# Performance work log

Hardware: AMD Instinct MI355X
Metric: run time of the kernel (lower is better)

The kernel has to match this reference:

```python
import jax, jax.numpy as jnp
import numpy as np

GROUPS = 32
EPS = 1e-5


def group_norm(x, gamma, beta):
    B, C, D, H, W = x.shape
    xr = x.reshape(B, GROUPS, C // GROUPS, D, H, W)
    mean = xr.mean(axis=(2, 3, 4, 5), keepdims=True)
    var = xr.var(axis=(2, 3, 4, 5), keepdims=True)
    xn = (xr - mean) * jax.lax.rsqrt(var + EPS)
    xn = xn.reshape(B, C, D, H, W)
    return xn * gamma[None, :, None, None, None] + beta[None, :, None, None, None]


def conv1x1(h, w, b):
    # 1x1x1 Conv3d == channel matmul. w: [O, C], b: [O]
    return jnp.einsum('oc,bcdhw->bodhw', w, h) + b[None, :, None, None, None]


def setup_inputs() -> dict:
    key = jax.random.key(0)
    ks = jax.random.split(key, 10)
    B, C, D, H, W = 2, 128, 16, 16, 16
    x = jax.random.normal(ks[0], (B, C, D, H, W), dtype=jnp.float32)
    gn_w = jnp.ones((C,), dtype=jnp.float32)
    gn_b = jnp.zeros((C,), dtype=jnp.float32)
    # xavier_uniform for [C, C, 1, 1, 1] conv: fan_in = fan_out = C
    lim = float(np.sqrt(6.0 / (C + C)))
    wq = jax.random.uniform(ks[1], (C, C), jnp.float32, -lim, lim)
    wk = jax.random.uniform(ks[2], (C, C), jnp.float32, -lim, lim)
    wv = jax.random.uniform(ks[3], (C, C), jnp.float32, -lim, lim)
    wp = jax.random.uniform(ks[4], (C, C), jnp.float32, -lim, lim) * 1e-05
    bq = jnp.zeros((C,), jnp.float32)
    bk = jnp.zeros((C,), jnp.float32)
    bv = jnp.zeros((C,), jnp.float32)
    bp = jnp.zeros((C,), jnp.float32)
    return {"x": x, "gn_w": gn_w, "gn_b": gn_b, "wq": wq, "bq": bq,
            "wk": wk, "bk": bk, "wv": wv, "bv": bv, "wp": wp, "bp": bp}


def reference(x, gn_w, gn_b, wq, bq, wk, bk, wv, bv, wp, bp):
    B, C, D, H, W = x.shape
    N = D * H * W
    h = group_norm(x, gn_w, gn_b)
    q = conv1x1(h, wq, bq)
    k = conv1x1(h, wk, bk)
    v = conv1x1(h, wv, bv)
    q = q.transpose(0, 2, 3, 4, 1).reshape(B, N, C)   # [B, N, C]
    k = k.reshape(B, C, N)                            # [B, C, N]
    v = v.transpose(0, 2, 3, 4, 1).reshape(B, N, C)   # [B, N, C]
    w = jnp.einsum('bnc,bcm->bnm', q, k) * (C ** -0.5)  # [B, N, N]
    w = jax.nn.softmax(w, axis=-1)
    h = jnp.einsum('bnm,bmc->bnc', w, v)              # [B, N, C]
    h = h.reshape(B, D, H, W, C).transpose(0, 4, 1, 2, 3)
    h = conv1x1(h, wp, bp)
    return x + h
```

## Files before the change

### kernel.cpp

```cpp
#include <hip/hip_runtime.h>
#include <math.h>

#define CC 128
#define NN 4096
#define BB 2
#define NGROUPS 32
#define CPG 4
#define GSIZE (CPG*NN)
#define KSPLIT 2

typedef __attribute__((ext_vector_type(8))) __bf16 bf16x8;
typedef __attribute__((ext_vector_type(4))) float floatx4;

__device__ __forceinline__ unsigned short f2bf(float f) {
  union { float f; unsigned u; } v; v.f = f;
  unsigned r = v.u + 0x7fff + ((v.u >> 16) & 1);
  return (unsigned short)(r >> 16);
}
__device__ __forceinline__ float bf2f(unsigned short u) {
  return __uint_as_float(((unsigned)u) << 16);
}


__global__ void gn_stats_kernel(const float* __restrict__ x, float2* __restrict__ stats) {
  int bid = blockIdx.x;
  int t = threadIdx.x;
  const float4* base = (const float4*)(x + (size_t)bid * 4096);
  float4 v = base[t];
  float s  = v.x + v.y + v.z + v.w;
  float ss = v.x*v.x + v.y*v.y + v.z*v.z + v.w*v.w;
  #pragma unroll
  for (int off = 1; off < 64; off <<= 1) {
    s  += __shfl_xor(s, off);
    ss += __shfl_xor(ss, off);
  }
  __shared__ float sred[4], ssred[4];
  if ((t & 63) == 0) { sred[t >> 6] = s; ssred[t >> 6] = ss; }
  __syncthreads();
  if (t == 0)
    stats[bid] = make_float2(sred[0]+sred[1]+sred[2]+sred[3],
                             ssred[0]+ssred[1]+ssred[2]+ssred[3]);
}

__global__ void prep_kernel(const float2* __restrict__ stats,
                            const float* __restrict__ gamma, const float* __restrict__ beta,
                            const float* __restrict__ wq, const float* __restrict__ bq,
                            const float* __restrict__ wk, const float* __restrict__ wv,
                            const float* __restrict__ wp,
                            float* __restrict__ ab_a, float* __restrict__ ab_b,
                            float* __restrict__ bqs,
                            unsigned short* __restrict__ wqb, unsigned short* __restrict__ wkb,
                            unsigned short* __restrict__ wvb, unsigned short* __restrict__ wpb) {
  const float sc = 0.08838834764831845f;
  int t = threadIdx.x;
  if (blockIdx.x == 64) {
    if (t < BB*NGROUPS) {
      float su = 0.f, ssq = 0.f;
      #pragma unroll
      for (int j = 0; j < 4; j++) { float2 p = stats[t*4 + j]; su += p.x; ssq += p.y; }
      float mean = su * (1.0f/GSIZE);
      float var  = ssq * (1.0f/GSIZE) - mean*mean;
      float rstd = rsqrtf(var + 1e-5f);
      int b = t / NGROUPS, g = t % NGROUPS;
      #pragma unroll
      for (int j = 0; j < 4; j++) {
        int c = g*4 + j;
        float a = rstd * gamma[c];
        ab_a[b*CC + c] = a;
        ab_b[b*CC + c] = beta[c] - mean * a;
      }
    }
    if (t < CC) bqs[t] = bq[t] * sc;
  } else {
    int i = blockIdx.x * 256 + t;
    int id = i >> 12, local = i & 4095;
    const float* src = id==0 ? wq : id==1 ? wk : id==2 ? wv : wp;
    unsigned short* dst = id==0 ? wqb : id==1 ? wkb : id==2 ? wvb : wpb;
    float s = (id == 0) ? sc : 1.0f;
    float4 v = ((const float4*)src)[local];
    unsigned p0 = (unsigned)f2bf(v.x*s) | ((unsigned)f2bf(v.y*s) << 16);
    unsigned p1 = (unsigned)f2bf(v.z*s) | ((unsigned)f2bf(v.w*s) << 16);
    ((uint2*)dst)[local] = make_uint2(p0, p1);
  }
}

__global__ __launch_bounds__(256, 2) void qkv_kernel(
    const float* __restrict__ x,
    const float* __restrict__ ab_a, const float* __restrict__ ab_b,
    const unsigned short* __restrict__ wqb, const unsigned short* __restrict__ wkb,
    const unsigned short* __restrict__ wvb,
    const float* __restrict__ bqs, const float* __restrict__ bk, const float* __restrict__ bv,
    unsigned short* __restrict__ q, unsigned short* __restrict__ k, unsigned short* __restrict__ v) {
  int z = blockIdx.z, b = blockIdx.y, n0 = blockIdx.x * 32;
  const unsigned short* wsel = z==0 ? wqb : z==1 ? wkb : wvb;
  const float* bias          = z==0 ? bqs : z==1 ? bk  : bv;
  unsigned short* outp       = z==0 ? q   : z==1 ? k   : v;
  __shared__ unsigned short hs[32][130];
  __shared__ unsigned short vs[32][136];
  int t = threadIdx.x;
  #pragma unroll
  for (int j = 0; j < 16; j++) {
    int idx = j*256 + t;
    int c = idx >> 5, n = idx & 31;
    float xv = x[((size_t)b*CC + c)*NN + n0 + n];
    hs[n][c] = f2bf(ab_a[b*CC + c]*xv + ab_b[b*CC + c]);
  }
  __syncthreads();
  int w = t >> 6, lane = t & 63, quad = lane >> 4, c = lane & 15;
  int o0 = w * 32;
  floatx4 acc[2][2];
  #pragma unroll
  for (int rt = 0; rt < 2; rt++)
    #pragma unroll
    for (int ct = 0; ct < 2; ct++) acc[rt][ct] = (floatx4){0.f,0.f,0.f,0.f};
  #pragma unroll
  for (int ks = 0; ks < 4; ks++) {
    bf16x8 af[2];
    af[0] = *(const bf16x8*)&hs[c     ][ks*32 + quad*8];
    af[1] = *(const bf16x8*)&hs[16 + c][ks*32 + quad*8];
    #pragma unroll
    for (int ct = 0; ct < 2; ct++) {
      bf16x8 bfr = *(const bf16x8*)(wsel + (size_t)(o0 + ct*16 + c)*CC + ks*32 + quad*8);
      acc[0][ct] = __builtin_amdgcn_mfma_f32_16x16x32_bf16(af[0], bfr, acc[0][ct], 0, 0, 0);
      acc[1][ct] = __builtin_amdgcn_mfma_f32_16x16x32_bf16(af[1], bfr, acc[1][ct], 0, 0, 0);
    }
  }
  if (z < 2) {
    size_t base = (size_t)b*NN*CC + ((size_t)(n0 >> 4))*2048 + w*512;
    #pragma unroll
    for (int ct = 0; ct < 2; ct++) {
      float bi = bias[o0 + ct*16 + c];
      #pragma unroll
      for (int rt = 0; rt < 2; rt++)
        #pragma unroll
        for (int r = 0; r < 4; r++)
          outp[base + rt*2048 + (quad*4 + r)*32 + ct*16 + c] = f2bf(acc[rt][ct][r] + bi);
    }
  } else {
    #pragma unroll
    for (int ct = 0; ct < 2; ct++) {
      float bi = bias[o0 + ct*16 + c];
      #pragma unroll
      for (int rt = 0; rt < 2; rt++)
        #pragma unroll
        for (int r = 0; r < 4; r++)
          vs[rt*16 + quad*4 + r][o0 + ct*16 + c] = f2bf(acc[rt][ct][r] + bi);
    }
    __syncthreads();
    int ct = t >> 5;
    int rem = t & 31;
    int c16 = rem >> 1;
    int m0 = (rem & 1) * 16;
    int ch = ct*16 + c16;
    unsigned pk[8];
    #pragma unroll
    for (int j2 = 0; j2 < 8; j2++) {
      unsigned lo = vs[m0 + j2*2    ][ch];
      unsigned hi = vs[m0 + j2*2 + 1][ch];
      pk[j2] = lo | (hi << 16);
    }
    uint4* dst = (uint4*)(outp + (size_t)b*NN*CC + ((size_t)(n0 >> 5))*4096 + ct*512 + c16*32 + m0);
    dst[0] = make_uint4(pk[0], pk[1], pk[2], pk[3]);
    dst[1] = make_uint4(pk[4], pk[5], pk[6], pk[7]);
  }
}

__global__ __launch_bounds__(256, 2) void attn_kernel(
    const unsigned short* __restrict__ qm,
    const unsigned short* __restrict__ km,
    const unsigned short* __restrict__ vm,
    unsigned short* __restrict__ Opart,
    float* __restrict__ lpart) {
  int b    = blockIdx.z;
  int kh   = blockIdx.y;
  int row0 = blockIdx.x * 32;
  int t    = threadIdx.x;
  int w    = t >> 6, lane = t & 63, quad = lane >> 4, c = lane & 15;

  __shared__ unsigned short shmem[4][32][132];
  __shared__ float lred[4][32];
  unsigned short (*Pl)[72] = (unsigned short (*)[72])&shmem[w][0][0];

  int fragoff = c*32 + quad*8;

  bf16x8 qa[2][4];
  const unsigned short* qbase = qm + (size_t)b*NN*CC + ((size_t)(row0 >> 4))*2048;
  #pragma unroll
  for (int rt = 0; rt < 2; rt++)
    #pragma unroll
    for (int ks = 0; ks < 4; ks++)
      qa[rt][ks] = *(const bf16x8*)(qbase + rt*2048 + ks*512 + fragoff);

  floatx4 O[2][8];
  #pragma unroll
  for (int rt = 0; rt < 2; rt++)
    #pragma unroll
    for (int ct = 0; ct < 8; ct++) O[rt][ct] = (floatx4){0.f,0.f,0.f,0.f};
  float lsum[2][4];
  #pragma unroll
  for (int rt = 0; rt < 2; rt++)
    #pragma unroll
    for (int r = 0; r < 4; r++) lsum[rt][r] = 0.f;

  const unsigned short* kb0 = km + (size_t)b*NN*CC;
  const unsigned short* vb0 = vm + (size_t)b*NN*CC;

  for (int it = 0; it < NN/KSPLIT/256; it++) {
    int mbase = kh*(NN/KSPLIT) + it*256 + w*64;
    const unsigned short* kt = kb0 + ((size_t)(mbase >> 4))*2048;
    const unsigned short* vt = vb0 + ((size_t)(mbase >> 5))*4096;
    floatx4 S[2][4];
    #pragma unroll
    for (int rt = 0; rt < 2; rt++)
      #pragma unroll
      for (int ct = 0; ct < 4; ct++) S[rt][ct] = (floatx4){0.f,0.f,0.f,0.f};
    #pragma unroll
    for (int ks = 0; ks < 4; ks++) {
      #pragma unroll
      for (int ct = 0; ct < 4; ct++) {
        bf16x8 kf = *(const bf16x8*)(kt + ct*2048 + ks*512 + fragoff);
        S[0][ct] = __builtin_amdgcn_mfma_f32_16x16x32_bf16(qa[0][ks], kf, S[0][ct], 0, 0, 0);
        S[1][ct] = __builtin_amdgcn_mfma_f32_16x16x32_bf16(qa[1][ks], kf, S[1][ct], 0, 0, 0);
      }
    }
    #pragma unroll
    for (int rt = 0; rt < 2; rt++) {
      #pragma unroll
      for (int ct = 0; ct < 4; ct++) {
        float e0 = __expf(S[rt][ct][0]);
        float e1 = __expf(S[rt][ct][1]);
        float e2 = __expf(S[rt][ct][2]);
        float e3 = __expf(S[rt][ct][3]);
        lsum[rt][0] += e0; lsum[rt][1] += e1;
        lsum[rt][2] += e2; lsum[rt][3] += e3;
        bool odd = (c & 1);
        float s01 = odd ? e0 : e1;
        float g01 = __shfl_xor(s01, 1);
        unsigned lo0 = __float_as_uint(odd ? g01 : e0);
        unsigned hi0 = __float_as_uint(odd ? e1 : g01);
        unsigned p0 = (hi0 & 0xffff0000u) | (lo0 >> 16);
        float s23 = odd ? e2 : e3;
        float g23 = __shfl_xor(s23, 1);
        unsigned lo1 = __float_as_uint(odd ? g23 : e2);
        unsigned hi1 = __float_as_uint(odd ? e3 : g23);
        unsigned p1 = (hi1 & 0xffff0000u) | (lo1 >> 16);
        int colpair = ct*16 + (c & ~1);
        int rowA = rt*16 + quad*4 + (odd ? 1 : 0);
        int rowB = rt*16 + quad*4 + (odd ? 3 : 2);
        *(unsigned*)&Pl[rowA][colpair] = p0;
        *(unsigned*)&Pl[rowB][colpair] = p1;
      }
    }
    #pragma unroll
    for (int ks2 = 0; ks2 < 2; ks2++) {
      bf16x8 pa0 = *(const bf16x8*)(&Pl[c     ][ks2*32 + quad*8]);
      bf16x8 pa1 = *(const bf16x8*)(&Pl[16 + c][ks2*32 + quad*8]);
      #pragma unroll
      for (int ct = 0; ct < 8; ct++) {
        bf16x8 vf = *(const bf16x8*)(vt + ks2*4096 + ct*512 + fragoff);
        O[0][ct] = __builtin_amdgcn_mfma_f32_16x16x32_bf16(pa0, vf, O[0][ct], 0, 0, 0);
        O[1][ct] = __builtin_amdgcn_mfma_f32_16x16x32_bf16(pa1, vf, O[1][ct], 0, 0, 0);
      }
    }
  }

  #pragma unroll
  for (int rt = 0; rt < 2; rt++)
    #pragma unroll
    for (int r = 0; r < 4; r++) {
      float vsum = lsum[rt][r];
      vsum += __shfl_xor(vsum, 1);
      vsum += __shfl_xor(vsum, 2);
      vsum += __shfl_xor(vsum, 4);
      vsum += __shfl_xor(vsum, 8);
      if (c == 0) lred[w][rt*16 + quad*4 + r] = vsum;
    }
  __syncthreads();
  #pragma unroll
  for (int rt = 0; rt < 2; rt++)
    #pragma unroll
    for (int ct = 0; ct < 8; ct++)
      #pragma unroll
      for (int r = 0; r < 4; r++)
        shmem[w][rt*16 + quad*4 + r][ct*16 + c] = f2bf(O[rt][ct][r]);
  __syncthreads();
  size_t pbase = (size_t)(kh*BB + b)*NN + row0;
  if (t < 32)
    lpart[pbase + t] = lred[0][t] + lred[1][t] + lred[2][t] + lred[3][t];
  int rr = t >> 3, c0 = (t & 7) * 16;
  unsigned pk[8];
  #pragma unroll
  for (int j2 = 0; j2 < 8; j2++) {
    int cc0 = c0 + j2*2;
    float v0 = bf2f(shmem[0][rr][cc0])   + bf2f(shmem[1][rr][cc0])
             + bf2f(shmem[2][rr][cc0])   + bf2f(shmem[3][rr][cc0]);
    float v1 = bf2f(shmem[0][rr][cc0+1]) + bf2f(shmem[1][rr][cc0+1])
             + bf2f(shmem[2][rr][cc0+1]) + bf2f(shmem[3][rr][cc0+1]);
    pk[j2] = (unsigned)f2bf(v0) | ((unsigned)f2bf(v1) << 16);
  }
  uint4* od = (uint4*)(Opart + (pbase + rr)*CC + c0);
  od[0] = make_uint4(pk[0], pk[1], pk[2], pk[3]);
  od[1] = make_uint4(pk[4], pk[5], pk[6], pk[7]);
}

__global__ __launch_bounds__(256, 2) void combine_kernel(
    const unsigned short* __restrict__ Opart, const float* __restrict__ lpart,
    const unsigned short* __restrict__ wpb, const float* __restrict__ bp,
    const float* __restrict__ x, float* __restrict__ out) {
  int b = blockIdx.y, n0 = blockIdx.x * 32;
  int t = threadIdx.x;
  __shared__ unsigned short hs[32][130];
  __shared__ float ps[32][132];
  __shared__ float linv[32];
  if (t < 32) {
    float l = 0.f;
    #pragma unroll
    for (int kh = 0; kh < KSPLIT; kh++)
      l += lpart[((size_t)(kh*BB + b))*NN + n0 + t];
    linv[t] = 1.f / l;
  }
  __syncthreads();
  #pragma unroll
  for (int j = 0; j < 16; j++) {
    int idx = j*256 + t;
    int n = idx >> 7, c2 = idx & 127;
    float o = 0.f;
    #pragma unroll
    for (int kh = 0; kh < KSPLIT; kh++)
      o += bf2f(Opart[((size_t)(kh*BB + b)*NN + n0 + n)*CC + c2]);
    hs[n][c2] = f2bf(o * linv[n]);
  }
  __syncthreads();
  int w = t >> 6, lane = t & 63, quad = lane >> 4, c = lane & 15;
  int o0 = w * 32;
  floatx4 acc[2][2];
  #pragma unroll
  for (int rt = 0; rt < 2; rt++)
    #pragma unroll
    for (int ct = 0; ct < 2; ct++) acc[rt][ct] = (floatx4){0.f,0.f,0.f,0.f};
  #pragma unroll
  for (int ks = 0; ks < 4; ks++) {
    bf16x8 af[2];
    af[0] = *(const bf16x8*)&hs[c     ][ks*32 + quad*8];
    af[1] = *(const bf16x8*)&hs[16 + c][ks*32 + quad*8];
    #pragma unroll
    for (int ct = 0; ct < 2; ct++) {
      bf16x8 bfr = *(const bf16x8*)(wpb + (size_t)(o0 + ct*16 + c)*CC + ks*32 + quad*8);
      acc[0][ct] = __builtin_amdgcn_mfma_f32_16x16x32_bf16(af[0], bfr, acc[0][ct], 0, 0, 0);
      acc[1][ct] = __builtin_amdgcn_mfma_f32_16x16x32_bf16(af[1], bfr, acc[1][ct], 0, 0, 0);
    }
  }
  #pragma unroll
  for (int rt = 0; rt < 2; rt++)
    #pragma unroll
    for (int ct = 0; ct < 2; ct++)
      #pragma unroll
      for (int r = 0; r < 4; r++)
        ps[rt*16 + quad*4 + r][o0 + ct*16 + c] = acc[rt][ct][r];
  __syncthreads();
  int o = t >> 1, nh = (t & 1) * 16;
  float bi = bp[o];
  const float* xr = x + ((size_t)b*CC + o)*NN + n0 + nh;
  float* orow = out + ((size_t)b*CC + o)*NN + n0 + nh;
  #pragma unroll
  for (int j4 = 0; j4 < 4; j4++) {
    float4 xv = ((const float4*)xr)[j4];
    float4 ov;
    ov.x = xv.x + ps[nh + j4*4 + 0][o] + bi;
    ov.y = xv.y + ps[nh + j4*4 + 1][o] + bi;
    ov.z = xv.z + ps[nh + j4*4 + 2][o] + bi;
    ov.w = xv.w + ps[nh + j4*4 + 3][o] + bi;
    ((float4*)orow)[j4] = ov;
  }
}

extern "C" void kernel_launch(void* const* d_in, const int* in_sizes, int n_in,
                              void* d_out, int out_size, void* d_ws, size_t ws_size,
                              hipStream_t stream) {
  const float* x    = (const float*)d_in[0];
  const float* gn_w = (const float*)d_in[1];
  const float* gn_b = (const float*)d_in[2];
  const float* wq   = (const float*)d_in[3];
  const float* bq   = (const float*)d_in[4];
  const float* wk   = (const float*)d_in[5];
  const float* bk   = (const float*)d_in[6];
  const float* wv   = (const float*)d_in[7];
  const float* bv   = (const float*)d_in[8];
  const float* wp   = (const float*)d_in[9];
  const float* bp   = (const float*)d_in[10];
  float* out = (float*)d_out;

  char* ws = (char*)d_ws;
  float2*         stats = (float2*)(ws);
  float*          ab_a  = (float*)(ws + 2048);
  float*          ab_b  = (float*)(ws + 3072);
  float*          bqs   = (float*)(ws + 4096);
  unsigned short* wqb   = (unsigned short*)(ws + 8192);
  unsigned short* wkb   = (unsigned short*)(ws + 8192 + 32768);
  unsigned short* wvb   = (unsigned short*)(ws + 8192 + 65536);
  unsigned short* wpb   = (unsigned short*)(ws + 8192 + 98304);
  unsigned short* qb    = (unsigned short*)(ws + 262144);
  unsigned short* kb    = (unsigned short*)(ws + 262144 + 2097152);
  unsigned short* vb    = (unsigned short*)(ws + 262144 + 2*2097152);
  unsigned short* Opart = (unsigned short*)(ws + 262144 + 3*2097152);
  float*          lpart = (float*)(ws + 262144 + 3*2097152 + 4194304);

  gn_stats_kernel<<<dim3(256), 256, 0, stream>>>(x, stats);
  prep_kernel    <<<dim3(65), 256, 0, stream>>>(stats, gn_w, gn_b, wq, bq, wk, wv, wp,
                                                ab_a, ab_b, bqs, wqb, wkb, wvb, wpb);
  qkv_kernel     <<<dim3(NN/32, BB, 3), 256, 0, stream>>>(x, ab_a, ab_b, wqb, wkb, wvb,
                                                          bqs, bk, bv, qb, kb, vb);
  attn_kernel    <<<dim3(NN/32, KSPLIT, BB), 256, 0, stream>>>(qb, kb, vb, Opart, lpart);
  combine_kernel <<<dim3(NN/32, BB), 256, 0, stream>>>(Opart, lpart, wpb, bp, x, out);
}
```

Before: 134.6 us.

## Raise attention key split, fold weight conversion into stats kernel, simplify P store

Raises the key-dimension split of the attention kernel from 2 to 4, giving more blocks across the GPU, and enlarges the partial-output workspace to match. Weight bf16 conversion moves into the group-norm stats kernel so it runs alongside the stats blocks, and prep shrinks to one block. The softmax probability write to shared memory drops the shuffle-based pairing and writes each bf16 element directly. The trade-offs are more partial outputs for the combine step to merge and narrower 16-bit LDS stores in the attention inner loop.

```diff
diff --git a/kernel.cpp b/kernel.cpp
--- a/kernel.cpp
+++ b/kernel.cpp
@@ -7,7 +7,7 @@
 #define NGROUPS 32
 #define CPG 4
 #define GSIZE (CPG*NN)
-#define KSPLIT 2
+#define KSPLIT 4
 
 typedef __attribute__((ext_vector_type(8))) __bf16 bf16x8;
 typedef __attribute__((ext_vector_type(4))) float floatx4;
@@ -22,57 +22,32 @@
 }
 
 
-__global__ void gn_stats_kernel(const float* __restrict__ x, float2* __restrict__ stats) {
-  int bid = blockIdx.x;
+__global__ void gn_stats_kernel(const float* __restrict__ x, float2* __restrict__ stats,
+                                const float* __restrict__ wq, const float* __restrict__ wk,
+                                const float* __restrict__ wv, const float* __restrict__ wp,
+                                unsigned short* __restrict__ wqb, unsigned short* __restrict__ wkb,
+                                unsigned short* __restrict__ wvb, unsigned short* __restrict__ wpb) {
   int t = threadIdx.x;
-  const float4* base = (const float4*)(x + (size_t)bid * 4096);
-  float4 v = base[t];
-  float s  = v.x + v.y + v.z + v.w;
-  float ss = v.x*v.x + v.y*v.y + v.z*v.z + v.w*v.w;
-  #pragma unroll
-  for (int off = 1; off < 64; off <<= 1) {
-    s  += __shfl_xor(s, off);
-    ss += __shfl_xor(ss, off);
-  }
-  __shared__ float sred[4], ssred[4];
-  if ((t & 63) == 0) { sred[t >> 6] = s; ssred[t >> 6] = ss; }
-  __syncthreads();
-  if (t == 0)
-    stats[bid] = make_float2(sred[0]+sred[1]+sred[2]+sred[3],
-                             ssred[0]+ssred[1]+ssred[2]+ssred[3]);
-}
-
-__global__ void prep_kernel(const float2* __restrict__ stats,
-                            const float* __restrict__ gamma, const float* __restrict__ beta,
-                            const float* __restrict__ wq, const float* __restrict__ bq,
-                            const float* __restrict__ wk, const float* __restrict__ wv,
-                            const float* __restrict__ wp,
-                            float* __restrict__ ab_a, float* __restrict__ ab_b,
-                            float* __restrict__ bqs,
-                            unsigned short* __restrict__ wqb, unsigned short* __restrict__ wkb,
-                            unsigned short* __restrict__ wvb, unsigned short* __restrict__ wpb) {
-  const float sc = 0.08838834764831845f;
-  int t = threadIdx.x;
-  if (blockIdx.x == 64) {
-    if (t < BB*NGROUPS) {
-      float su = 0.f, ssq = 0.f;
-      #pragma unroll
-      for (int j = 0; j < 4; j++) { float2 p = stats[t*4 + j]; su += p.x; ssq += p.y; }
-      float mean = su * (1.0f/GSIZE);
-      float var  = ssq * (1.0f/GSIZE) - mean*mean;
-      float rstd = rsqrtf(var + 1e-5f);
-      int b = t / NGROUPS, g = t % NGROUPS;
-      #pragma unroll
-      for (int j = 0; j < 4; j++) {
-        int c = g*4 + j;
-        float a = rstd * gamma[c];
-        ab_a[b*CC + c] = a;
-        ab_b[b*CC + c] = beta[c] - mean * a;
-      }
-    }
-    if (t < CC) bqs[t] = bq[t] * sc;
+  if (blockIdx.x < 256) {
+    int bid = blockIdx.x;
+    const float4* base = (const float4*)(x + (size_t)bid * 4096);
+    float4 v = base[t];
+    float s  = v.x + v.y + v.z + v.w;
+    float ss = v.x*v.x + v.y*v.y + v.z*v.z + v.w*v.w;
+    #pragma unroll
+    for (int off = 1; off < 64; off <<= 1) {
+      s  += __shfl_xor(s, off);
+      ss += __shfl_xor(ss, off);
+    }
+    __shared__ float sred[4], ssred[4];
+    if ((t & 63) == 0) { sred[t >> 6] = s; ssred[t >> 6] = ss; }
+    __syncthreads();
+    if (t == 0)
+      stats[bid] = make_float2(sred[0]+sred[1]+sred[2]+sred[3],
+                               ssred[0]+ssred[1]+ssred[2]+ssred[3]);
   } else {
-    int i = blockIdx.x * 256 + t;
+    const float sc = 0.08838834764831845f;
+    int i = (blockIdx.x - 256) * 256 + t;
     int id = i >> 12, local = i & 4095;
     const float* src = id==0 ? wq : id==1 ? wk : id==2 ? wv : wp;
     unsigned short* dst = id==0 ? wqb : id==1 ? wkb : id==2 ? wvb : wpb;
@@ -82,6 +57,32 @@
     unsigned p1 = (unsigned)f2bf(v.z*s) | ((unsigned)f2bf(v.w*s) << 16);
     ((uint2*)dst)[local] = make_uint2(p0, p1);
   }
+}
+
+__global__ void prep_kernel(const float2* __restrict__ stats,
+                            const float* __restrict__ gamma, const float* __restrict__ beta,
+                            const float* __restrict__ bq,
+                            float* __restrict__ ab_a, float* __restrict__ ab_b,
+                            float* __restrict__ bqs) {
+  const float sc = 0.08838834764831845f;
+  int t = threadIdx.x;
+  if (t < BB*NGROUPS) {
+    float su = 0.f, ssq = 0.f;
+    #pragma unroll
+    for (int j = 0; j < 4; j++) { float2 p = stats[t*4 + j]; su += p.x; ssq += p.y; }
+    float mean = su * (1.0f/GSIZE);
+    float var  = ssq * (1.0f/GSIZE) - mean*mean;
+    float rstd = rsqrtf(var + 1e-5f);
+    int b = t / NGROUPS, g = t % NGROUPS;
+    #pragma unroll
+    for (int j = 0; j < 4; j++) {
+      int c = g*4 + j;
+      float a = rstd * gamma[c];
+      ab_a[b*CC + c] = a;
+      ab_b[b*CC + c] = beta[c] - mean * a;
+    }
+  }
+  if (t < CC) bqs[t] = bq[t] * sc;
 }
 
 __global__ __launch_bounds__(256, 2) void qkv_kernel(
@@ -227,28 +228,12 @@
     for (int rt = 0; rt < 2; rt++) {
       #pragma unroll
       for (int ct = 0; ct < 4; ct++) {
-        float e0 = __expf(S[rt][ct][0]);
-        float e1 = __expf(S[rt][ct][1]);
-        float e2 = __expf(S[rt][ct][2]);
-        float e3 = __expf(S[rt][ct][3]);
-        lsum[rt][0] += e0; lsum[rt][1] += e1;
-        lsum[rt][2] += e2; lsum[rt][3] += e3;
-        bool odd = (c & 1);
-        float s01 = odd ? e0 : e1;
-        float g01 = __shfl_xor(s01, 1);
-        unsigned lo0 = __float_as_uint(odd ? g01 : e0);
-        unsigned hi0 = __float_as_uint(odd ? e1 : g01);
-        unsigned p0 = (hi0 & 0xffff0000u) | (lo0 >> 16);
-        float s23 = odd ? e2 : e3;
-        float g23 = __shfl_xor(s23, 1);
-        unsigned lo1 = __float_as_uint(odd ? g23 : e2);
-        unsigned hi1 = __float_as_uint(odd ? e3 : g23);
-        unsigned p1 = (hi1 & 0xffff0000u) | (lo1 >> 16);
-        int colpair = ct*16 + (c & ~1);
-        int rowA = rt*16 + quad*4 + (odd ? 1 : 0);
-        int rowB = rt*16 + quad*4 + (odd ? 3 : 2);
-        *(unsigned*)&Pl[rowA][colpair] = p0;
-        *(unsigned*)&Pl[rowB][colpair] = p1;
+        #pragma unroll
+        for (int r = 0; r < 4; r++) {
+          float e = __expf(S[rt][ct][r]);
+          lsum[rt][r] += e;
+          Pl[rt*16 + quad*4 + r][ct*16 + c] = (unsigned short)(__float_as_uint(e) >> 16);
+        }
       }
     }
     #pragma unroll
@@ -403,11 +388,11 @@
   unsigned short* kb    = (unsigned short*)(ws + 262144 + 2097152);
   unsigned short* vb    = (unsigned short*)(ws + 262144 + 2*2097152);
   unsigned short* Opart = (unsigned short*)(ws + 262144 + 3*2097152);
-  float*          lpart = (float*)(ws + 262144 + 3*2097152 + 4194304);
-
-  gn_stats_kernel<<<dim3(256), 256, 0, stream>>>(x, stats);
-  prep_kernel    <<<dim3(65), 256, 0, stream>>>(stats, gn_w, gn_b, wq, bq, wk, wv, wp,
-                                                ab_a, ab_b, bqs, wqb, wkb, wvb, wpb);
+  float*          lpart = (float*)(ws + 262144 + 3*2097152 + 8388608);
+
+  gn_stats_kernel<<<dim3(320), 256, 0, stream>>>(x, stats, wq, wk, wv, wp,
+                                                 wqb, wkb, wvb, wpb);
+  prep_kernel    <<<dim3(1), 256, 0, stream>>>(stats, gn_w, gn_b, bq, ab_a, ab_b, bqs);
   qkv_kernel     <<<dim3(NN/32, BB, 3), 256, 0, stream>>>(x, ab_a, ab_b, wqb, wkb, wvb,
                                                           bqs, bk, bv, qb, kb, vb);
   attn_kernel    <<<dim3(NN/32, KSPLIT, BB), 256, 0, stream>>>(qb, kb, vb, Opart, lpart);
```

After: 155.0 us. 15.2% more time.
